# Performance work log

Measured on AMD Instinct MI355X. Metric: run time of the kernel, lower is better.

## Reference

```python
import jax, jax.numpy as jnp
import numpy as np

DIM = 512
HEADS = 8
WINDOW = 128


def setup_inputs() -> dict:
    key = jax.random.key(0)
    k1, k2, k3, k4 = jax.random.split(key, 4)
    x = jax.random.normal(k1, (16, 4096, DIM), dtype=jnp.float32)
    w_qkv = jax.random.normal(k2, (3 * DIM, DIM), dtype=jnp.float32) * 0.02
    w_proj = jax.random.normal(k3, (DIM, DIM), dtype=jnp.float32) * 0.02
    b_proj = jax.random.normal(k4, (DIM,), dtype=jnp.float32) * 0.02
    return {"x": x, "w_qkv": w_qkv, "w_proj": w_proj, "b_proj": b_proj}


def reference(x, w_qkv, w_proj, b_proj):
    B0, T0, C = x.shape
    H = HEADS
    hd = C // H
    scale = hd ** (-0.5)
    W = WINDOW
    # split into independent windows: [B*T/W, W, C]
    xw = x.reshape(-1, W, C)
    Bw = xw.shape[0]
    # qkv projection (no bias), reshape to [3, Bw, H, W, hd]
    qkv = (xw @ w_qkv.T).reshape(Bw, W, 3, H, hd).transpose(2, 0, 3, 1, 4)
    q, k, v = qkv[0], qkv[1], qkv[2]
    # scaled scores per window: [Bw, H, W, W]
    attn = jnp.einsum("bhqd,bhkd->bhqk", q, k) * scale
    causal_mask = jnp.tril(jnp.ones((W, W), dtype=bool))
    attn = jnp.where(causal_mask, attn, -jnp.inf)
    attn = jax.nn.softmax(attn, axis=-1)
    out = jnp.einsum("bhqk,bhkd->bhqd", attn, v)  # [Bw, H, W, hd]
    out = out.transpose(0, 2, 1, 3).reshape(Bw, W, C)
    out = out @ w_proj.T + b_proj
    return out.reshape(B0, T0, C)
```

## Files before the change

### kernel.cpp

```cpp
#include <hip/hip_runtime.h>
#include <stdint.h>


typedef unsigned short ushort_t;
typedef __attribute__((ext_vector_type(8))) short short8;
typedef __attribute__((ext_vector_type(4))) float f32x4;
typedef __attribute__((ext_vector_type(4))) float f4v;
typedef __attribute__((ext_vector_type(4))) unsigned short us4;

static __device__ __forceinline__ unsigned short f2bf(float f) {
  unsigned int u = __float_as_uint(f);
  u += 0x7FFFu + ((u >> 16) & 1u);
  return (unsigned short)(u >> 16);
}

static __device__ __forceinline__ void gl_lds16(const ushort_t* g, ushort_t* l) {
  __builtin_amdgcn_global_load_lds(
      (const __attribute__((address_space(1))) void*)g,
      (__attribute__((address_space(3))) void*)l, 16, 0, 0);
}

__global__ __launch_bounds__(256) void cast_f32_bf16(const float* __restrict__ in,
                                                     ushort_t* __restrict__ out, int n4) {
  int i = blockIdx.x * 256 + threadIdx.x;
  if (i >= n4) return;
  f4v v = ((const f4v*)in)[i];
  us4 o;
  o.x = f2bf(v.x); o.y = f2bf(v.y); o.z = f2bf(v.z); o.w = f2bf(v.w);
  ((us4*)out)[i] = o;
}

__global__ __launch_bounds__(512, 2) void qkv_gemm(const ushort_t* __restrict__ A,
                                                   const ushort_t* __restrict__ B,
                                                   ushort_t* __restrict__ q_ws,
                                                   ushort_t* __restrict__ k_ws,
                                                   ushort_t* __restrict__ vT) {
  __shared__ __align__(16) ushort_t smem[3 * 24576];
  const int tid = threadIdx.x;
  const int lane = tid & 63;
  const int wv = tid >> 6;
  const int wr = wv >> 1, wc = wv & 1;
  const int lr = lane & 15;
  const int lg = lane >> 4;

  const int bid = blockIdx.x;
  const int wg = (bid & 7) * 384 + (bid >> 3);
  const int nb = wg % 12;
  const int mb = wg / 12;
  const int m0 = mb << 8;
  const int n0 = nb << 7;

  const int srow = tid >> 3;
  const int ssw  = (((tid & 7) ^ (srow & 7)) << 3);
  const ushort_t* gA = A + (size_t)(m0 + srow) * 512 + ssw;
  const ushort_t* gB = B + (size_t)(n0 + srow) * 512 + ssw;

  f32x4 acc[4][4] = {};

  auto STAGE = [&](int t, int q) {
    ushort_t* Ab = smem + q * 24576;
    ushort_t* Bb = Ab + 16384;
    const int kk = t << 6;
#pragma unroll
    for (int r = 0; r < 4; ++r)
      gl_lds16(gA + (size_t)(r * 64) * 512 + kk, Ab + (r * 512 + wv * 64) * 8);
#pragma unroll
    for (int r = 0; r < 2; ++r)
      gl_lds16(gB + (size_t)(r * 64) * 512 + kk, Bb + (r * 512 + wv * 64) * 8);
  };

  STAGE(0, 0);
  STAGE(1, 1);
  asm volatile("s_waitcnt vmcnt(6)" ::: "memory");
  __builtin_amdgcn_s_barrier();

#pragma unroll
  for (int t = 0; t < 8; ++t) {
    const ushort_t* Ab = smem + (t % 3) * 24576;
    const ushort_t* Bb = Ab + 16384;
    short8 a[4][2], b[4][2];
#pragma unroll
    for (int ks = 0; ks < 2; ++ks) {
      const int co = ((((ks << 2) | lg) ^ (lr & 7)) << 3);
#pragma unroll
      for (int mi = 0; mi < 4; ++mi)
        a[mi][ks] = *(const short8*)(Ab + (wr * 64 + mi * 16 + lr) * 64 + co);
#pragma unroll
      for (int ni = 0; ni < 4; ++ni)
        b[ni][ks] = *(const short8*)(Bb + (wc * 64 + ni * 16 + lr) * 64 + co);
    }
    if (t + 2 < 8) STAGE(t + 2, (t + 2) % 3);
    if (t < 7) {
      if (t + 2 < 8) asm volatile("s_waitcnt vmcnt(6)" ::: "memory");
      else           asm volatile("s_waitcnt vmcnt(0)" ::: "memory");
      asm volatile("s_waitcnt lgkmcnt(0)" ::: "memory");
      __builtin_amdgcn_s_barrier();
    }
    __builtin_amdgcn_s_setprio(1);
#pragma unroll
    for (int ks = 0; ks < 2; ++ks)
#pragma unroll
      for (int mi = 0; mi < 4; ++mi)
#pragma unroll
        for (int ni = 0; ni < 4; ++ni)
          acc[mi][ni] = __builtin_amdgcn_mfma_f32_16x16x32_bf16(a[mi][ks], b[ni][ks], acc[mi][ni], 0, 0, 0);
    __builtin_amdgcn_s_setprio(0);
  }

  const int lg4 = lg << 2;
  if (n0 < 1024) {
    ushort_t* dst = (n0 < 512) ? q_ws : k_ws;
    const int cbase = (n0 < 512) ? n0 : (n0 - 512);
#pragma unroll
    for (int mi = 0; mi < 4; ++mi) {
      const int rr0 = wr * 64 + mi * 16 + lg4;
#pragma unroll
      for (int ni = 0; ni < 4; ++ni) {
        const int c = cbase + wc * 64 + ni * 16 + lr;
        const int h = c >> 6, d = c & 63;
#pragma unroll
        for (int rg = 0; rg < 4; ++rg) {
          const int rr = rr0 + rg;
          const int win = (m0 >> 7) + (rr >> 7);
          dst[(size_t)(win * 8 + h) * 8192 + (rr & 127) * 64 + d] = f2bf(acc[mi][ni][rg]);
        }
      }
    }
  } else {
    const int winb = (m0 >> 7) + (wr >> 1);
    const int t0b = (wr & 1) * 64;
#pragma unroll
    for (int mi = 0; mi < 4; ++mi) {
      const int t0 = t0b + mi * 16 + lg4;
#pragma unroll
      for (int ni = 0; ni < 4; ++ni) {
        const int c = n0 - 1024 + wc * 64 + ni * 16 + lr;
        const int h = c >> 6, d = c & 63;
        us4 o;
        o.x = f2bf(acc[mi][ni][0]); o.y = f2bf(acc[mi][ni][1]);
        o.z = f2bf(acc[mi][ni][2]); o.w = f2bf(acc[mi][ni][3]);
        *(us4*)(vT + (size_t)((winb * 8 + h) * 64 + d) * 128 + t0) = o;
      }
    }
  }
}

__global__ __launch_bounds__(256) void attn_kernel(const ushort_t* __restrict__ q_ws,
                                                   const ushort_t* __restrict__ k_ws,
                                                   const ushort_t* __restrict__ vT,
                                                   ushort_t* __restrict__ attn_out) {
  __shared__ __align__(16) ushort_t smem[24576];
  ushort_t* ks_ = smem;
  ushort_t* vs = smem + 8192;

  const int tid = threadIdx.x;
  const int lane = tid & 63;
  const int wv = tid >> 6;
  const int win = blockIdx.x >> 3;
  const int h = blockIdx.x & 7;
  const int lr = lane & 15;
  const int lg = lane >> 4;
  const int lg4 = lg << 2;
  const int sw = lr & 7;

  const size_t base = (size_t)(win * 8 + h) * 8192;

#pragma unroll
  for (int i = 0; i < 4; ++i) {
    const int g = i * 256 + tid;
    const int t = g >> 3, ch = g & 7;
    gl_lds16(k_ws + base + t * 64 + ((ch ^ (t & 7)) << 3), ks_ + g * 8);
    const int d = g >> 4, ch2 = g & 15;
    gl_lds16(vT + base + d * 128 + ((ch2 ^ (d & 7)) << 3), vs + g * 8);
  }

  const int rt[2] = {wv, 7 - wv};

  short8 aq[2][2];
#pragma unroll
  for (int mi = 0; mi < 2; ++mi)
#pragma unroll
    for (int ks = 0; ks < 2; ++ks)
      aq[mi][ks] = *(const short8*)(q_ws + base + (size_t)(rt[mi] * 16 + lr) * 64 + ks * 32 + lg * 8);

  __syncthreads();

  f32x4 sacc[2][8] = {};
#pragma unroll
  for (int ks2 = 0; ks2 < 2; ++ks2) {
    const int co = ((((ks2 << 2) | lg) ^ sw) << 3);
#pragma unroll
    for (int ni = 0; ni < 8; ++ni) {
      if (ni <= rt[1]) {
        short8 b = *(const short8*)(ks_ + (ni * 16 + lr) * 64 + co);
        if (ni <= rt[0])
          sacc[0][ni] = __builtin_amdgcn_mfma_f32_16x16x32_bf16(aq[0][ks2], b, sacc[0][ni], 0, 0, 0);
        sacc[1][ni] = __builtin_amdgcn_mfma_f32_16x16x32_bf16(aq[1][ks2], b, sacc[1][ni], 0, 0, 0);
      }
    }
  }

  __syncthreads();

  const float C = 0.125f * 1.44269504f;
#pragma unroll
  for (int mi = 0; mi < 2; ++mi) {
    const int r = rt[mi];
    const int rb = r * 16;
#pragma unroll
    for (int ni = 0; ni < 8; ++ni) {
      if (ni <= r) {
#pragma unroll
        for (int rg = 0; rg < 4; ++rg) {
          const int row = rb + lg4 + rg;
          const int col = ni * 16 + lr;
          float e = __builtin_exp2f(sacc[mi][ni][rg] * C);
          e = (col <= row) ? e : 0.0f;
          smem[(row & 63) * 128 + ((row >> 6) << 14) +
               ((((col >> 3) ^ (row & 7)) << 3) | (col & 7))] = f2bf(e);
        }
      }
    }
    if (!(r & 1)) {
      const int col = (r + 1) * 16 + lr;
#pragma unroll
      for (int rg = 0; rg < 4; ++rg) {
        const int row = rb + lg4 + rg;
        smem[(row & 63) * 128 + ((row >> 6) << 14) +
             ((((col >> 3) ^ (row & 7)) << 3) | (col & 7))] = 0;
      }
    }
  }

  const short one_bf = (short)0x3F80;
  short8 ones;
#pragma unroll
  for (int j = 0; j < 8; ++j) ones[j] = (lr == 0) ? one_bf : (short)0;

  const int r0 = rt[0] * 16 + lr;
  const int r1 = rt[1] * 16 + lr;
  const ushort_t* p0 = smem + (r0 & 63) * 128 + ((r0 >> 6) << 14);
  const ushort_t* p1 = smem + (r1 & 63) * 128 + ((r1 >> 6) << 14);

  f32x4 oacc[2][4] = {};
  f32x4 sm[2] = {};
#pragma unroll
  for (int ks2 = 0; ks2 < 4; ++ks2) {
    const int co = ((((ks2 << 2) | lg) ^ sw) << 3);
    if (ks2 <= (rt[1] >> 1)) {
      short8 b[4];
#pragma unroll
      for (int nd = 0; nd < 4; ++nd)
        b[nd] = *(const short8*)(vs + (nd * 16 + lr) * 128 + co);
      short8 a1 = *(const short8*)(p1 + co);
#pragma unroll
      for (int nd = 0; nd < 4; ++nd)
        oacc[1][nd] = __builtin_amdgcn_mfma_f32_16x16x32_bf16(a1, b[nd], oacc[1][nd], 0, 0, 0);
      sm[1] = __builtin_amdgcn_mfma_f32_16x16x32_bf16(a1, ones, sm[1], 0, 0, 0);
      if (ks2 <= (rt[0] >> 1)) {
        short8 a0 = *(const short8*)(p0 + co);
#pragma unroll
        for (int nd = 0; nd < 4; ++nd)
          oacc[0][nd] = __builtin_amdgcn_mfma_f32_16x16x32_bf16(a0, b[nd], oacc[0][nd], 0, 0, 0);
        sm[0] = __builtin_amdgcn_mfma_f32_16x16x32_bf16(a0, ones, sm[0], 0, 0, 0);
      }
    }
  }

  const int src = lane & 48;
  const size_t obase = (size_t)win * 128 * 512 + h * 64;
#pragma unroll
  for (int mi = 0; mi < 2; ++mi) {
    const int rb = rt[mi] * 16;
    float rsv[4];
#pragma unroll
    for (int rg = 0; rg < 4; ++rg)
      rsv[rg] = 1.0f / __shfl(sm[mi][rg], src);
#pragma unroll
    for (int nd = 0; nd < 4; ++nd)
#pragma unroll
      for (int rg = 0; rg < 4; ++rg) {
        const int row = rb + lg4 + rg;
        const int col = nd * 16 + lr;
        attn_out[obase + (size_t)row * 512 + col] = f2bf(oacc[mi][nd][rg] * rsv[rg]);
      }
  }
}

__global__ __launch_bounds__(512, 2) void proj_gemm(const ushort_t* __restrict__ A,
                                                    const ushort_t* __restrict__ B,
                                                    const float* __restrict__ bias,
                                                    float* __restrict__ out) {
  __shared__ __align__(16) ushort_t smem[3 * 24576];
  const int tid = threadIdx.x;
  const int lane = tid & 63;
  const int wv = tid >> 6;
  const int wr = wv >> 1, wc = wv & 1;
  const int lr = lane & 15;
  const int lg = lane >> 4;

  const int bid = blockIdx.x;
  const int wg = (bid & 7) * 128 + (bid >> 3);
  const int nb = wg & 3;
  const int mb = wg >> 2;
  const int m0 = mb << 8;
  const int n0 = nb << 7;

  const int srow = tid >> 3;
  const int ssw  = (((tid & 7) ^ (srow & 7)) << 3);
  const ushort_t* gA = A + (size_t)(m0 + srow) * 512 + ssw;
  const ushort_t* gB = B + (size_t)(n0 + srow) * 512 + ssw;

  f32x4 acc[4][4] = {};

  auto STAGE = [&](int t, int q) {
    ushort_t* Ab = smem + q * 24576;
    ushort_t* Bb = Ab + 16384;
    const int kk = t << 6;
#pragma unroll
    for (int r = 0; r < 4; ++r)
      gl_lds16(gA + (size_t)(r * 64) * 512 + kk, Ab + (r * 512 + wv * 64) * 8);
#pragma unroll
    for (int r = 0; r < 2; ++r)
      gl_lds16(gB + (size_t)(r * 64) * 512 + kk, Bb + (r * 512 + wv * 64) * 8);
  };

  STAGE(0, 0);
  STAGE(1, 1);
  asm volatile("s_waitcnt vmcnt(6)" ::: "memory");
  __builtin_amdgcn_s_barrier();

#pragma unroll
  for (int t = 0; t < 8; ++t) {
    const ushort_t* Ab = smem + (t % 3) * 24576;
    const ushort_t* Bb = Ab + 16384;
    short8 a[4][2], b[4][2];
#pragma unroll
    for (int ks = 0; ks < 2; ++ks) {
      const int co = ((((ks << 2) | lg) ^ (lr & 7)) << 3);
#pragma unroll
      for (int mi = 0; mi < 4; ++mi)
        a[mi][ks] = *(const short8*)(Ab + (wr * 64 + mi * 16 + lr) * 64 + co);
#pragma unroll
      for (int ni = 0; ni < 4; ++ni)
        b[ni][ks] = *(const short8*)(Bb + (wc * 64 + ni * 16 + lr) * 64 + co);
    }
    if (t + 2 < 8) STAGE(t + 2, (t + 2) % 3);
    if (t < 7) {
      if (t + 2 < 8) asm volatile("s_waitcnt vmcnt(6)" ::: "memory");
      else           asm volatile("s_waitcnt vmcnt(0)" ::: "memory");
      asm volatile("s_waitcnt lgkmcnt(0)" ::: "memory");
      __builtin_amdgcn_s_barrier();
    }
    __builtin_amdgcn_s_setprio(1);
#pragma unroll
    for (int ks = 0; ks < 2; ++ks)
#pragma unroll
      for (int mi = 0; mi < 4; ++mi)
#pragma unroll
        for (int ni = 0; ni < 4; ++ni)
          acc[mi][ni] = __builtin_amdgcn_mfma_f32_16x16x32_bf16(a[mi][ks], b[ni][ks], acc[mi][ni], 0, 0, 0);
    __builtin_amdgcn_s_setprio(0);
  }

  const int lg4 = lg << 2;
#pragma unroll
  for (int mi = 0; mi < 4; ++mi) {
    const int rbase = m0 + wr * 64 + mi * 16 + lg4;
#pragma unroll
    for (int ni = 0; ni < 4; ++ni) {
      const int col = n0 + wc * 64 + ni * 16 + lr;
      const float bv = bias[col];
#pragma unroll
      for (int rg = 0; rg < 4; ++rg)
        out[(size_t)(rbase + rg) * 512 + col] = acc[mi][ni][rg] + bv;
    }
  }
}

extern "C" void kernel_launch(void* const* d_in, const int* in_sizes, int n_in,
                              void* d_out, int out_size, void* d_ws, size_t ws_size,
                              hipStream_t stream) {
  const float* x      = (const float*)d_in[0];
  const float* w_qkv  = (const float*)d_in[1];
  const float* w_proj = (const float*)d_in[2];
  const float* b_proj = (const float*)d_in[3];
  float* out = (float*)d_out;

  char* ws = (char*)d_ws;
  ushort_t* x_bf     = (ushort_t*)(ws);
  ushort_t* q_ws     = (ushort_t*)(ws + 67108864);
  ushort_t* k_ws     = (ushort_t*)(ws + 134217728);
  ushort_t* vT_ws    = (ushort_t*)(ws + 201326592);
  ushort_t* attn_ws  = (ushort_t*)(ws + 268435456);
  ushort_t* wqkv_bf  = (ushort_t*)(ws + 335544320);
  ushort_t* wproj_bf = (ushort_t*)(ws + 337117184);

  cast_f32_bf16<<<32768, 256, 0, stream>>>(x, x_bf, 8388608);
  cast_f32_bf16<<<768, 256, 0, stream>>>(w_qkv, wqkv_bf, 196608);
  cast_f32_bf16<<<256, 256, 0, stream>>>(w_proj, wproj_bf, 65536);

  qkv_gemm<<<3072, 512, 0, stream>>>(x_bf, wqkv_bf, q_ws, k_ws, vT_ws);
  attn_kernel<<<4096, 256, 0, stream>>>(q_ws, k_ws, vT_ws, attn_ws);
  proj_gemm<<<1024, 512, 0, stream>>>(attn_ws, wproj_bf, b_proj, out);
}
```

Baseline: 480.4 us.

## Widen cast kernel, read V directly from global, simplify proj GEMM tiling

Three unrelated changes are bundled. The cast kernel now converts 8 floats per thread with a 16-byte store instead of 4. The attention kernel stops staging V^T in LDS and reads its fragments straight from global memory, shrinking LDS. The projection GEMM drops the triple-buffered 512-thread pipeline for a simpler single-buffer 256-thread 128x128 tile with barriers each k-step. This aims for higher occupancy, but it gives up load/compute overlap in proj and adds uncoalesced global reads for V.

```diff
diff --git a/kernel.cpp b/kernel.cpp
--- a/kernel.cpp
+++ b/kernel.cpp
@@ -4,6 +4,7 @@
 
 typedef unsigned short ushort_t;
 typedef __attribute__((ext_vector_type(8))) short short8;
+typedef __attribute__((ext_vector_type(8))) unsigned short us8;
 typedef __attribute__((ext_vector_type(4))) float f32x4;
 typedef __attribute__((ext_vector_type(4))) float f4v;
 typedef __attribute__((ext_vector_type(4))) unsigned short us4;
@@ -21,13 +22,15 @@
 }
 
 __global__ __launch_bounds__(256) void cast_f32_bf16(const float* __restrict__ in,
-                                                     ushort_t* __restrict__ out, int n4) {
+                                                     ushort_t* __restrict__ out, int n8) {
   int i = blockIdx.x * 256 + threadIdx.x;
-  if (i >= n4) return;
-  f4v v = ((const f4v*)in)[i];
-  us4 o;
-  o.x = f2bf(v.x); o.y = f2bf(v.y); o.z = f2bf(v.z); o.w = f2bf(v.w);
-  ((us4*)out)[i] = o;
+  if (i >= n8) return;
+  f4v v0 = ((const f4v*)in)[2 * i];
+  f4v v1 = ((const f4v*)in)[2 * i + 1];
+  us8 o;
+  o[0] = f2bf(v0.x); o[1] = f2bf(v0.y); o[2] = f2bf(v0.z); o[3] = f2bf(v0.w);
+  o[4] = f2bf(v1.x); o[5] = f2bf(v1.y); o[6] = f2bf(v1.z); o[7] = f2bf(v1.w);
+  ((us8*)out)[i] = o;
 }
 
 __global__ __launch_bounds__(512, 2) void qkv_gemm(const ushort_t* __restrict__ A,
@@ -149,9 +152,8 @@
                                                    const ushort_t* __restrict__ k_ws,
                                                    const ushort_t* __restrict__ vT,
                                                    ushort_t* __restrict__ attn_out) {
-  __shared__ __align__(16) ushort_t smem[24576];
+  __shared__ __align__(16) ushort_t smem[16384];
   ushort_t* ks_ = smem;
-  ushort_t* vs = smem + 8192;
 
   const int tid = threadIdx.x;
   const int lane = tid & 63;
@@ -170,8 +172,6 @@
     const int g = i * 256 + tid;
     const int t = g >> 3, ch = g & 7;
     gl_lds16(k_ws + base + t * 64 + ((ch ^ (t & 7)) << 3), ks_ + g * 8);
-    const int d = g >> 4, ch2 = g & 15;
-    gl_lds16(vT + base + d * 128 + ((ch2 ^ (d & 7)) << 3), vs + g * 8);
   }
 
   const int rt[2] = {wv, 7 - wv};
@@ -216,7 +216,7 @@
           const int col = ni * 16 + lr;
           float e = __builtin_exp2f(sacc[mi][ni][rg] * C);
           e = (col <= row) ? e : 0.0f;
-          smem[(row & 63) * 128 + ((row >> 6) << 14) +
+          smem[(row & 63) * 128 + ((row >> 6) << 13) +
                ((((col >> 3) ^ (row & 7)) << 3) | (col & 7))] = f2bf(e);
         }
       }
@@ -226,7 +226,7 @@
 #pragma unroll
       for (int rg = 0; rg < 4; ++rg) {
         const int row = rb + lg4 + rg;
-        smem[(row & 63) * 128 + ((row >> 6) << 14) +
+        smem[(row & 63) * 128 + ((row >> 6) << 13) +
              ((((col >> 3) ^ (row & 7)) << 3) | (col & 7))] = 0;
       }
     }
@@ -239,19 +239,21 @@
 
   const int r0 = rt[0] * 16 + lr;
   const int r1 = rt[1] * 16 + lr;
-  const ushort_t* p0 = smem + (r0 & 63) * 128 + ((r0 >> 6) << 14);
-  const ushort_t* p1 = smem + (r1 & 63) * 128 + ((r1 >> 6) << 14);
+  const ushort_t* p0 = smem + (r0 & 63) * 128 + ((r0 >> 6) << 13);
+  const ushort_t* p1 = smem + (r1 & 63) * 128 + ((r1 >> 6) << 13);
+  const ushort_t* vg = vT + base;
 
   f32x4 oacc[2][4] = {};
   f32x4 sm[2] = {};
 #pragma unroll
   for (int ks2 = 0; ks2 < 4; ++ks2) {
     const int co = ((((ks2 << 2) | lg) ^ sw) << 3);
+    const int cv = (((ks2 << 2) | lg) << 3);
     if (ks2 <= (rt[1] >> 1)) {
       short8 b[4];
 #pragma unroll
       for (int nd = 0; nd < 4; ++nd)
-        b[nd] = *(const short8*)(vs + (nd * 16 + lr) * 128 + co);
+        b[nd] = *(const short8*)(vg + (size_t)(nd * 16 + lr) * 128 + cv);
       short8 a1 = *(const short8*)(p1 + co);
 #pragma unroll
       for (int nd = 0; nd < 4; ++nd)
@@ -287,80 +289,58 @@
   }
 }
 
-__global__ __launch_bounds__(512, 2) void proj_gemm(const ushort_t* __restrict__ A,
-                                                    const ushort_t* __restrict__ B,
-                                                    const float* __restrict__ bias,
-                                                    float* __restrict__ out) {
-  __shared__ __align__(16) ushort_t smem[3 * 24576];
+__global__ __launch_bounds__(256) void proj_gemm(const ushort_t* __restrict__ A,
+                                                 const ushort_t* __restrict__ B,
+                                                 const float* __restrict__ bias,
+                                                 float* __restrict__ out) {
+  __shared__ __align__(16) ushort_t As[128 * 64];
+  __shared__ __align__(16) ushort_t Bs[128 * 64];
   const int tid = threadIdx.x;
   const int lane = tid & 63;
   const int wv = tid >> 6;
   const int wr = wv >> 1, wc = wv & 1;
   const int lr = lane & 15;
   const int lg = lane >> 4;
+  const int sw = lr & 7;
 
   const int bid = blockIdx.x;
-  const int wg = (bid & 7) * 128 + (bid >> 3);
+  const int wg = (bid & 7) * 256 + (bid >> 3);
   const int nb = wg & 3;
   const int mb = wg >> 2;
-  const int m0 = mb << 8;
+  const int m0 = mb << 7;
   const int n0 = nb << 7;
 
-  const int srow = tid >> 3;
-  const int ssw  = (((tid & 7) ^ (srow & 7)) << 3);
-  const ushort_t* gA = A + (size_t)(m0 + srow) * 512 + ssw;
-  const ushort_t* gB = B + (size_t)(n0 + srow) * 512 + ssw;
-
   f32x4 acc[4][4] = {};
 
-  auto STAGE = [&](int t, int q) {
-    ushort_t* Ab = smem + q * 24576;
-    ushort_t* Bb = Ab + 16384;
-    const int kk = t << 6;
-#pragma unroll
-    for (int r = 0; r < 4; ++r)
-      gl_lds16(gA + (size_t)(r * 64) * 512 + kk, Ab + (r * 512 + wv * 64) * 8);
-#pragma unroll
-    for (int r = 0; r < 2; ++r)
-      gl_lds16(gB + (size_t)(r * 64) * 512 + kk, Bb + (r * 512 + wv * 64) * 8);
-  };
-
-  STAGE(0, 0);
-  STAGE(1, 1);
-  asm volatile("s_waitcnt vmcnt(6)" ::: "memory");
-  __builtin_amdgcn_s_barrier();
-
-#pragma unroll
-  for (int t = 0; t < 8; ++t) {
-    const ushort_t* Ab = smem + (t % 3) * 24576;
-    const ushort_t* Bb = Ab + 16384;
-    short8 a[4][2], b[4][2];
+  const int grow = tid >> 3;
+  const int gcol = (((tid & 7) ^ (grow & 7)) << 3);
+  const ushort_t* gA = A + (size_t)(m0 + grow) * 512 + gcol;
+  const ushort_t* gB = B + (size_t)(n0 + grow) * 512 + gcol;
+
+  for (int kk = 0; kk < 512; kk += 64) {
+#pragma unroll
+    for (int r = 0; r < 4; ++r) {
+      gl_lds16(gA + (size_t)(r * 32) * 512 + kk, As + (size_t)(r * 256 + wv * 64) * 8);
+      gl_lds16(gB + (size_t)(r * 32) * 512 + kk, Bs + (size_t)(r * 256 + wv * 64) * 8);
+    }
+    __syncthreads();
 #pragma unroll
     for (int ks = 0; ks < 2; ++ks) {
-      const int co = ((((ks << 2) | lg) ^ (lr & 7)) << 3);
+      const int co = ((((ks << 2) | lg) ^ sw) << 3);
+      short8 a[4], b[4];
 #pragma unroll
       for (int mi = 0; mi < 4; ++mi)
-        a[mi][ks] = *(const short8*)(Ab + (wr * 64 + mi * 16 + lr) * 64 + co);
+        a[mi] = *(const short8*)(As + (wr * 64 + mi * 16 + lr) * 64 + co);
 #pragma unroll
       for (int ni = 0; ni < 4; ++ni)
-        b[ni][ks] = *(const short8*)(Bb + (wc * 64 + ni * 16 + lr) * 64 + co);
-    }
-    if (t + 2 < 8) STAGE(t + 2, (t + 2) % 3);
-    if (t < 7) {
-      if (t + 2 < 8) asm volatile("s_waitcnt vmcnt(6)" ::: "memory");
-      else           asm volatile("s_waitcnt vmcnt(0)" ::: "memory");
-      asm volatile("s_waitcnt lgkmcnt(0)" ::: "memory");
-      __builtin_amdgcn_s_barrier();
-    }
-    __builtin_amdgcn_s_setprio(1);
-#pragma unroll
-    for (int ks = 0; ks < 2; ++ks)
+        b[ni] = *(const short8*)(Bs + (wc * 64 + ni * 16 + lr) * 64 + co);
 #pragma unroll
       for (int mi = 0; mi < 4; ++mi)
 #pragma unroll
         for (int ni = 0; ni < 4; ++ni)
-          acc[mi][ni] = __builtin_amdgcn_mfma_f32_16x16x32_bf16(a[mi][ks], b[ni][ks], acc[mi][ni], 0, 0, 0);
-    __builtin_amdgcn_s_setprio(0);
+          acc[mi][ni] = __builtin_amdgcn_mfma_f32_16x16x32_bf16(a[mi], b[ni], acc[mi][ni], 0, 0, 0);
+    }
+    __syncthreads();
   }
 
   const int lg4 = lg << 2;
@@ -396,11 +376,11 @@
   ushort_t* wqkv_bf  = (ushort_t*)(ws + 335544320);
   ushort_t* wproj_bf = (ushort_t*)(ws + 337117184);
 
-  cast_f32_bf16<<<32768, 256, 0, stream>>>(x, x_bf, 8388608);
-  cast_f32_bf16<<<768, 256, 0, stream>>>(w_qkv, wqkv_bf, 196608);
-  cast_f32_bf16<<<256, 256, 0, stream>>>(w_proj, wproj_bf, 65536);
+  cast_f32_bf16<<<16384, 256, 0, stream>>>(x, x_bf, 4194304);
+  cast_f32_bf16<<<384, 256, 0, stream>>>(w_qkv, wqkv_bf, 98304);
+  cast_f32_bf16<<<128, 256, 0, stream>>>(w_proj, wproj_bf, 32768);
 
   qkv_gemm<<<3072, 512, 0, stream>>>(x_bf, wqkv_bf, q_ws, k_ws, vT_ws);
   attn_kernel<<<4096, 256, 0, stream>>>(q_ws, k_ws, vT_ws, attn_ws);
-  proj_gemm<<<1024, 512, 0, stream>>>(attn_ws, wproj_bf, b_proj, out);
-}
+  proj_gemm<<<2048, 256, 0, stream>>>(attn_ws, wproj_bf, b_proj, out);
+}
```

Result: slower. 509.6 us (+6.1%).
